# Kernel optimization log

Measured on AMD Instinct MI355X. Metric: run time of the kernel, lower is better.

Reference implementation:

```python
import jax, jax.numpy as jnp
import numpy as np


def setup_inputs() -> dict:
    key = jax.random.key(0)
    k1, k2 = jax.random.split(key)
    B, N, M, D = 8, 8192, 8192, 3
    gts = jax.random.normal(k1, (B, N, D), dtype=jnp.float32)
    preds = jax.random.normal(k2, (B, M, D), dtype=jnp.float32)
    return {"gts": gts, "preds": preds}


def reference(gts, preds):
    # Chamfer distance (pytorch3d defaults): squared L2, mean over points,
    # mean over batch, sum of both directions.
    x2 = jnp.sum(gts * gts, axis=-1)          # [B, N]
    y2 = jnp.sum(preds * preds, axis=-1)      # [B, M]
    xy = jnp.einsum('bnd,bmd->bnm', gts, preds)  # [B, N, M]
    d2 = x2[:, :, None] + y2[:, None, :] - 2.0 * xy
    d2 = jnp.maximum(d2, 0.0)  # guard tiny negative values from cancellation
    cham_x = jnp.mean(jnp.min(d2, axis=2))  # x -> nearest y, mean over N then B
    cham_y = jnp.mean(jnp.min(d2, axis=1))  # y -> nearest x, mean over M then B
    return cham_x + cham_y
```

## Files before the change

kernel.cpp:

```cpp
#include <hip/hip_runtime.h>
#include <hip/hip_bf16.h>
#include <math.h>


#define BLOCK 256
#define WAVES 4
#define QPW 64
#define NCHUNK 2

typedef short short8 __attribute__((ext_vector_type(8)));
typedef float f32x16 __attribute__((ext_vector_type(16)));

union U16S { uint4 v; short8 s; };

__device__ __forceinline__ unsigned int bf16hi(float f) {
    __hip_bfloat16 h = __float2bfloat16(f);
    return (unsigned int)*reinterpret_cast<unsigned short*>(&h);
}
__device__ __forceinline__ float bf16f(unsigned int u) {
    unsigned short us = (unsigned short)u;
    __hip_bfloat16 h;
    *reinterpret_cast<unsigned short*>(&h) = us;
    return __bfloat162float(h);
}

__device__ __forceinline__ f32x16 mfma_bf16(short8 a, short8 b, f32x16 c) {
    f32x16 d;
    asm volatile("v_mfma_f32_32x32x16_bf16 %0, %1, %2, %3"
                 : "=v"(d) : "v"(a), "v"(b), "v"(c));
    return d;
}
__device__ __forceinline__ void mfma_fence4(f32x16& a, f32x16& b, f32x16& c, f32x16& d) {
    asm volatile("s_nop 7\n\ts_nop 7" : "+v"(a), "+v"(b), "+v"(c), "+v"(d));
}

__global__ void prep_kernel(const float* __restrict__ gts, const float* __restrict__ preds,
                            int nG, int nP, uint4* __restrict__ recG, uint4* __restrict__ recP,
                            float* out) {
    const int idx = blockIdx.x * blockDim.x + threadIdx.x;
    if (idx == 0) out[0] = 0.0f;
    if (idx >= nG + nP) return;
    const float* src;
    uint4* dst;
    if (idx < nG) { src = gts + 3 * (size_t)idx;          dst = recG + idx; }
    else          { src = preds + 3 * (size_t)(idx - nG); dst = recP + (idx - nG); }
    const float x = src[0], y = src[1], z = src[2];
    const float w = -0.5f * (x * x + y * y + z * z);
    const unsigned int xh = bf16hi(x), yh = bf16hi(y), zh = bf16hi(z), wh = bf16hi(w);
    const unsigned int xl = bf16hi(x - bf16f(xh));
    const unsigned int yl = bf16hi(y - bf16f(yh));
    const unsigned int zl = bf16hi(z - bf16f(zh));
    const unsigned int wl = bf16hi(w - bf16f(wh));
    *dst = make_uint4(xh | (yh << 16), zh | (wh << 16),
                      xl | (yl << 16), zl | (wl << 16));
}

__global__ void __launch_bounds__(BLOCK, 4)
nn_kernel(const uint4* __restrict__ recG, const uint4* __restrict__ recP,
          float* __restrict__ kpart, int N, int M, int B) {
    const int z = blockIdx.z;
    const bool dirX = (z < B);
    const int b = dirX ? z : z - B;
    const int NQ = dirX ? N : M;
    const int NR = dirX ? M : N;
    const uint4* Qr = (dirX ? recG : recP) + (size_t)b * NQ;
    const uint4* Rr = (dirX ? recP : recG) + (size_t)b * NR;
    const int nGP = B * (N + M) / 2 * 2;
    float* outK = kpart + (size_t)blockIdx.y * nGP + (dirX ? 0 : B * N) + (size_t)b * NQ;

    const int tid = threadIdx.x;
    const int lane = tid & 63;
    const int wave = tid >> 6;
    const int m = lane & 31;
    const bool hiK = lane >= 32;
    const unsigned int loMask = hiK ? 0u : 0xFFFFFFFFu;
    const int qBase = (blockIdx.x * WAVES + wave) * QPW;

    const uint4 q0 = Qr[qBase + m];
    const uint4 q1 = Qr[qBase + 32 + m];
    U16S a;
    a.v.x = q0.x;
    a.v.y = (q0.y & 0xFFFFu) | 0x3F800000u;
    a.v.z = q0.z & loMask;
    a.v.w = q0.w & 0xFFFFu & loMask;
    const short8 A0 = a.s;
    a.v.x = q1.x;
    a.v.y = (q1.y & 0xFFFFu) | 0x3F800000u;
    a.v.z = q1.z & loMask;
    a.v.w = q1.w & 0xFFFFu & loMask;
    const short8 A1 = a.s;

    f32x16 zc;
    #pragma unroll
    for (int r = 0; r < 16; ++r) zc[r] = 0.0f;
    f32x16 k0, k1;
    #pragma unroll
    for (int r = 0; r < 16; ++r) { k0[r] = -INFINITY; k1[r] = -INFINITY; }

    const int chunk = NR / NCHUNK;
    const uint2* p = (const uint2*)(Rr + (size_t)blockIdx.y * chunk) + 2 * m + (hiK ? 1 : 0);
    const int iters = chunk / 64;

    uint2 t0 = p[0], t1 = p[64];
    #pragma unroll 1
    for (int it = 0; it < iters; ++it) {
        const uint2 n0 = p[128];
        const uint2 n1 = p[192];

        U16S b0, b1;
        b0.v.x = t0.x;          b0.v.y = t0.y;
        b0.v.z = t0.x & loMask; b0.v.w = t0.y & loMask;
        b1.v.x = t1.x;          b1.v.y = t1.y;
        b1.v.z = t1.x & loMask; b1.v.w = t1.y & loMask;

        f32x16 c0 = mfma_bf16(A0, b0.s, zc);
        f32x16 c1 = mfma_bf16(A1, b0.s, zc);
        f32x16 c2 = mfma_bf16(A0, b1.s, zc);
        f32x16 c3 = mfma_bf16(A1, b1.s, zc);
        mfma_fence4(c0, c1, c2, c3);
        #pragma unroll
        for (int r = 0; r < 16; ++r) {
            k0[r] = fmaxf(fmaxf(c0[r], c2[r]), k0[r]);
            k1[r] = fmaxf(fmaxf(c1[r], c3[r]), k1[r]);
        }

        t0 = n0; t1 = n1;
        p += 128;
    }

    __shared__ float sT[WAVES][64][36];
    #pragma unroll
    for (int r = 0; r < 16; ++r) {
        const int row = (r & 3) + 8 * (r >> 2) + 4 * (lane >> 5);
        sT[wave][row][m]      = k0[r];
        sT[wave][32 + row][m] = k1[r];
    }
    const float4* rowp = (const float4*)&sT[wave][lane][0];
    float4 m01 = rowp[0];
    #pragma unroll
    for (int kk = 1; kk < 8; ++kk) {
        const float4 t = rowp[kk];
        m01.x = fmaxf(m01.x, t.x); m01.y = fmaxf(m01.y, t.y);
        m01.z = fmaxf(m01.z, t.z); m01.w = fmaxf(m01.w, t.w);
    }
    const float cmax = fmaxf(fmaxf(m01.x, m01.y), fmaxf(m01.z, m01.w));
    outK[qBase + lane] = cmax;
}

__global__ void __launch_bounds__(BLOCK)
reduce_kernel(const float* __restrict__ kpart, const float* __restrict__ gts, int nG,
              const float* __restrict__ preds, int nP,
              float invx, float invy, float* __restrict__ out) {
    const int total = nG + nP;
    float local = 0.0f;
    for (int idx = blockIdx.x * blockDim.x + threadIdx.x; idx < total;
         idx += gridDim.x * blockDim.x) {
        const float c = fmaxf(kpart[idx], kpart[total + idx]);
        const float* q;
        float inv;
        if (idx < nG) { q = gts + 3 * (size_t)idx;          inv = invx; }
        else          { q = preds + 3 * (size_t)(idx - nG); inv = invy; }
        const float q2 = q[0] * q[0] + q[1] * q[1] + q[2] * q[2];
        local += fmaxf(q2 - 2.0f * c, 0.0f) * inv;
    }
    __shared__ float waveSums[BLOCK / 64];
    float v = local;
    #pragma unroll
    for (int off = 32; off; off >>= 1) v += __shfl_xor(v, off);
    if ((threadIdx.x & 63) == 0) waveSums[threadIdx.x >> 6] = v;
    __syncthreads();
    if (threadIdx.x == 0) {
        float s = 0.0f;
        #pragma unroll
        for (int w = 0; w < BLOCK / 64; ++w) s += waveSums[w];
        atomicAdd(out, s);
    }
}

extern "C" void kernel_launch(void* const* d_in, const int* in_sizes, int n_in,
                              void* d_out, int out_size, void* d_ws, size_t ws_size,
                              hipStream_t stream) {
    const float* gts   = (const float*)d_in[0];
    const float* preds = (const float*)d_in[1];
    float* out = (float*)d_out;

    const int B = 8;
    const int N = in_sizes[0] / (B * 3);
    const int M = in_sizes[1] / (B * 3);
    const int nG = B * N, nP = B * M;

    uint4* recG  = (uint4*)d_ws;
    uint4* recP  = recG + nG;
    float* kpart = (float*)(recP + nP);

    prep_kernel<<<(nG + nP + BLOCK - 1) / BLOCK, BLOCK, 0, stream>>>(
        gts, preds, nG, nP, recG, recP, out);

    dim3 grid(N / (WAVES * QPW), NCHUNK, 2 * B);
    nn_kernel<<<grid, BLOCK, 0, stream>>>(recG, recP, kpart, N, M, B);

    reduce_kernel<<<256, BLOCK, 0, stream>>>(
        kpart, gts, nG, preds, nP, 1.0f / (float)nG, 1.0f / (float)nP, out);
}
```

Before: 98.76 us.

## Restructure MFMA operand layout, vectorize prep, precompute norms for reduction

The A operand is rearranged so the high-K lanes carry the low-order bf16 parts of the query. Each B operand can then be the full 16-byte reference record loaded directly, with no per-iteration masking, and the main loop is unrolled by two with reloads interleaved. The prep kernel now handles four points per thread using float4 loads and also writes squared norms, so the reduction no longer re-reads and recomputes from the raw inputs. The wider per-lane loads double the load bytes per reference point, and the unroll assumes the iteration count is even.

```diff
diff --git a/kernel.cpp b/kernel.cpp
--- a/kernel.cpp
+++ b/kernel.cpp
@@ -36,23 +36,37 @@
 
 __global__ void prep_kernel(const float* __restrict__ gts, const float* __restrict__ preds,
                             int nG, int nP, uint4* __restrict__ recG, uint4* __restrict__ recP,
-                            float* out) {
-    const int idx = blockIdx.x * blockDim.x + threadIdx.x;
-    if (idx == 0) out[0] = 0.0f;
-    if (idx >= nG + nP) return;
+                            float* __restrict__ q2, float* out) {
+    const int t = blockIdx.x * blockDim.x + threadIdx.x;
+    if (t == 0) out[0] = 0.0f;
+    const int i0 = t * 4;
+    if (i0 >= nG + nP) return;
     const float* src;
-    uint4* dst;
-    if (idx < nG) { src = gts + 3 * (size_t)idx;          dst = recG + idx; }
-    else          { src = preds + 3 * (size_t)(idx - nG); dst = recP + (idx - nG); }
-    const float x = src[0], y = src[1], z = src[2];
-    const float w = -0.5f * (x * x + y * y + z * z);
-    const unsigned int xh = bf16hi(x), yh = bf16hi(y), zh = bf16hi(z), wh = bf16hi(w);
-    const unsigned int xl = bf16hi(x - bf16f(xh));
-    const unsigned int yl = bf16hi(y - bf16f(yh));
-    const unsigned int zl = bf16hi(z - bf16f(zh));
-    const unsigned int wl = bf16hi(w - bf16f(wh));
-    *dst = make_uint4(xh | (yh << 16), zh | (wh << 16),
-                      xl | (yl << 16), zl | (wl << 16));
+    uint4* rec;
+    if (i0 < nG) { src = gts + 3 * (size_t)i0;                rec = recG + i0; }
+    else         { src = preds + 3 * (size_t)(i0 - nG);       rec = recP + (i0 - nG); }
+    const float4 f0 = ((const float4*)src)[0];
+    const float4 f1 = ((const float4*)src)[1];
+    const float4 f2 = ((const float4*)src)[2];
+    const float xs[4] = {f0.x, f0.w, f1.z, f2.y};
+    const float ys[4] = {f0.y, f1.x, f1.w, f2.z};
+    const float zs[4] = {f0.z, f1.y, f2.x, f2.w};
+    float4 q2v;
+    #pragma unroll
+    for (int i = 0; i < 4; ++i) {
+        const float x = xs[i], y = ys[i], z = zs[i];
+        const float n2 = x * x + y * y + z * z;
+        ((float*)&q2v)[i] = n2;
+        const float w = -0.5f * n2;
+        const unsigned int xh = bf16hi(x), yh = bf16hi(y), zh = bf16hi(z), wh = bf16hi(w);
+        const unsigned int xl = bf16hi(x - bf16f(xh));
+        const unsigned int yl = bf16hi(y - bf16f(yh));
+        const unsigned int zl = bf16hi(z - bf16f(zh));
+        const unsigned int wl = bf16hi(w - bf16f(wh));
+        rec[i] = make_uint4(xh | (yh << 16), zh | (wh << 16),
+                            xl | (yl << 16), zl | (wl << 16));
+    }
+    ((float4*)q2)[t] = q2v;
 }
 
 __global__ void __launch_bounds__(BLOCK, 4)
@@ -65,7 +79,7 @@
     const int NR = dirX ? M : N;
     const uint4* Qr = (dirX ? recG : recP) + (size_t)b * NQ;
     const uint4* Rr = (dirX ? recP : recG) + (size_t)b * NR;
-    const int nGP = B * (N + M) / 2 * 2;
+    const int nGP = B * N + B * M;
     float* outK = kpart + (size_t)blockIdx.y * nGP + (dirX ? 0 : B * N) + (size_t)b * NQ;
 
     const int tid = threadIdx.x;
@@ -73,21 +87,20 @@
     const int wave = tid >> 6;
     const int m = lane & 31;
     const bool hiK = lane >= 32;
-    const unsigned int loMask = hiK ? 0u : 0xFFFFFFFFu;
     const int qBase = (blockIdx.x * WAVES + wave) * QPW;
 
     const uint4 q0 = Qr[qBase + m];
     const uint4 q1 = Qr[qBase + 32 + m];
     U16S a;
-    a.v.x = q0.x;
-    a.v.y = (q0.y & 0xFFFFu) | 0x3F800000u;
-    a.v.z = q0.z & loMask;
-    a.v.w = q0.w & 0xFFFFu & loMask;
+    a.v.x = hiK ? q0.z : q0.x;
+    a.v.y = hiK ? (q0.w & 0xFFFFu) : ((q0.y & 0xFFFFu) | 0x3F800000u);
+    a.v.z = hiK ? 0u : a.v.x;
+    a.v.w = hiK ? 0u : a.v.y;
     const short8 A0 = a.s;
-    a.v.x = q1.x;
-    a.v.y = (q1.y & 0xFFFFu) | 0x3F800000u;
-    a.v.z = q1.z & loMask;
-    a.v.w = q1.w & 0xFFFFu & loMask;
+    a.v.x = hiK ? q1.z : q1.x;
+    a.v.y = hiK ? (q1.w & 0xFFFFu) : ((q1.y & 0xFFFFu) | 0x3F800000u);
+    a.v.z = hiK ? 0u : a.v.x;
+    a.v.w = hiK ? 0u : a.v.y;
     const short8 A1 = a.s;
 
     f32x16 zc;
@@ -98,21 +111,12 @@
     for (int r = 0; r < 16; ++r) { k0[r] = -INFINITY; k1[r] = -INFINITY; }
 
     const int chunk = NR / NCHUNK;
-    const uint2* p = (const uint2*)(Rr + (size_t)blockIdx.y * chunk) + 2 * m + (hiK ? 1 : 0);
+    const uint4* p = Rr + (size_t)blockIdx.y * chunk + m;
     const int iters = chunk / 64;
 
-    uint2 t0 = p[0], t1 = p[64];
-    #pragma unroll 1
-    for (int it = 0; it < iters; ++it) {
-        const uint2 n0 = p[128];
-        const uint2 n1 = p[192];
-
+    auto computeSet = [&](uint4 ta, uint4 tb) {
         U16S b0, b1;
-        b0.v.x = t0.x;          b0.v.y = t0.y;
-        b0.v.z = t0.x & loMask; b0.v.w = t0.y & loMask;
-        b1.v.x = t1.x;          b1.v.y = t1.y;
-        b1.v.z = t1.x & loMask; b1.v.w = t1.y & loMask;
-
+        b0.v = ta; b1.v = tb;
         f32x16 c0 = mfma_bf16(A0, b0.s, zc);
         f32x16 c1 = mfma_bf16(A1, b0.s, zc);
         f32x16 c2 = mfma_bf16(A0, b1.s, zc);
@@ -123,8 +127,15 @@
             k0[r] = fmaxf(fmaxf(c0[r], c2[r]), k0[r]);
             k1[r] = fmaxf(fmaxf(c1[r], c3[r]), k1[r]);
         }
-
-        t0 = n0; t1 = n1;
+    };
+
+    uint4 t0 = p[0], t1 = p[32];
+    #pragma unroll 1
+    for (int it = 0; it < iters; it += 2) {
+        const uint4 u0 = p[64], u1 = p[96];
+        computeSet(t0, t1);
+        t0 = p[128]; t1 = p[160];
+        computeSet(u0, u1);
         p += 128;
     }
 
@@ -139,29 +150,24 @@
     float4 m01 = rowp[0];
     #pragma unroll
     for (int kk = 1; kk < 8; ++kk) {
-        const float4 t = rowp[kk];
-        m01.x = fmaxf(m01.x, t.x); m01.y = fmaxf(m01.y, t.y);
-        m01.z = fmaxf(m01.z, t.z); m01.w = fmaxf(m01.w, t.w);
+        const float4 tt = rowp[kk];
+        m01.x = fmaxf(m01.x, tt.x); m01.y = fmaxf(m01.y, tt.y);
+        m01.z = fmaxf(m01.z, tt.z); m01.w = fmaxf(m01.w, tt.w);
     }
     const float cmax = fmaxf(fmaxf(m01.x, m01.y), fmaxf(m01.z, m01.w));
     outK[qBase + lane] = cmax;
 }
 
 __global__ void __launch_bounds__(BLOCK)
-reduce_kernel(const float* __restrict__ kpart, const float* __restrict__ gts, int nG,
-              const float* __restrict__ preds, int nP,
-              float invx, float invy, float* __restrict__ out) {
+reduce_kernel(const float* __restrict__ kpart, const float* __restrict__ q2,
+              int nG, int nP, float invx, float invy, float* __restrict__ out) {
     const int total = nG + nP;
     float local = 0.0f;
     for (int idx = blockIdx.x * blockDim.x + threadIdx.x; idx < total;
          idx += gridDim.x * blockDim.x) {
         const float c = fmaxf(kpart[idx], kpart[total + idx]);
-        const float* q;
-        float inv;
-        if (idx < nG) { q = gts + 3 * (size_t)idx;          inv = invx; }
-        else          { q = preds + 3 * (size_t)(idx - nG); inv = invy; }
-        const float q2 = q[0] * q[0] + q[1] * q[1] + q[2] * q[2];
-        local += fmaxf(q2 - 2.0f * c, 0.0f) * inv;
+        const float inv = (idx < nG) ? invx : invy;
+        local += fmaxf(q2[idx] - 2.0f * c, 0.0f) * inv;
     }
     __shared__ float waveSums[BLOCK / 64];
     float v = local;
@@ -191,14 +197,15 @@
 
     uint4* recG  = (uint4*)d_ws;
     uint4* recP  = recG + nG;
-    float* kpart = (float*)(recP + nP);
-
-    prep_kernel<<<(nG + nP + BLOCK - 1) / BLOCK, BLOCK, 0, stream>>>(
-        gts, preds, nG, nP, recG, recP, out);
+    float* q2    = (float*)(recP + nP);
+    float* kpart = q2 + (nG + nP);
+
+    prep_kernel<<<((nG + nP) / 4 + BLOCK - 1) / BLOCK, BLOCK, 0, stream>>>(
+        gts, preds, nG, nP, recG, recP, q2, out);
 
     dim3 grid(N / (WAVES * QPW), NCHUNK, 2 * B);
     nn_kernel<<<grid, BLOCK, 0, stream>>>(recG, recP, kpart, N, M, B);
 
     reduce_kernel<<<256, BLOCK, 0, stream>>>(
-        kpart, gts, nG, preds, nP, 1.0f / (float)nG, 1.0f / (float)nP, out);
-}
+        kpart, q2, nG, nP, 1.0f / (float)nG, 1.0f / (float)nP, out);
+}
```

Result: slower. 238.0 us (+141.0%).
